# Optimization experiments

Measured on AMD Instinct MI355X. Metric: run time of the kernel, lower is better.

The kernel has to match this reference:

```python
import jax, jax.numpy as jnp
import numpy as np

WINDOW = 7
TOKEN_SELF_ATTN_VALUE = -5e4  # from lucidrains local-attention
LN_EPS = 1e-5


def _layer_norm(x, g, b):
    mu = jnp.mean(x, axis=-1, keepdims=True)
    var = jnp.mean(jnp.square(x - mu), axis=-1, keepdims=True)
    return (x - mu) * jax.lax.rsqrt(var + LN_EPS) * g + b


def _local_attention(q, k, v, window):
    # q,k,v: (b, n, d); shared_qk=True, causal=True, look_backward=1, look_forward=0
    b, n, d = q.shape
    nw = n // window
    scale = d ** -0.5
    # shared_qk: l2-normalize keys (torch F.normalize eps=1e-12)
    k = k / jnp.maximum(jnp.linalg.norm(k, axis=-1, keepdims=True), 1e-12)
    bq = q.reshape(b, nw, window, d) * scale
    bk = k.reshape(b, nw, window, d)
    bv = v.reshape(b, nw, window, d)
    # look_around: previous window + current window -> (b, nw, 2w, d)
    prev_k = jnp.pad(bk, ((0, 0), (1, 0), (0, 0), (0, 0)))[:, :nw]
    prev_v = jnp.pad(bv, ((0, 0), (1, 0), (0, 0), (0, 0)))[:, :nw]
    bk2 = jnp.concatenate([prev_k, bk], axis=2)
    bv2 = jnp.concatenate([prev_v, bv], axis=2)
    # absolute positions; padded positions marked -1
    t = jnp.arange(n).reshape(nw, window)             # (nw, w)
    prev_t = jnp.pad(t, ((1, 0), (0, 0)), constant_values=-1)[:nw]
    tk = jnp.concatenate([prev_t, t], axis=1)          # (nw, 2w)
    sim = jnp.einsum('bnie,bnje->bnij', bq, bk2)       # (b, nw, w, 2w)
    self_mask = t[:, :, None] == tk[:, None, :]
    sim = jnp.where(self_mask, TOKEN_SELF_ATTN_VALUE, sim)
    invalid = (t[:, :, None] < tk[:, None, :]) | (tk[:, None, :] == -1)
    sim = jnp.where(invalid, -jnp.finfo(sim.dtype).max, sim)
    attn = jax.nn.softmax(sim, axis=-1)
    out = jnp.einsum('bnij,bnjd->bnid', attn, bv2)
    return out.reshape(b, n, d)


def setup_inputs() -> dict:
    key = jax.random.key(0)
    ks = jax.random.split(key, 10)
    B, H, W, C = 8, 112, 112, 256
    s = 1.0 / np.sqrt(C)
    return {
        'x': jax.random.normal(ks[0], (B, H, W, C), dtype=jnp.float32),
        'ln_g': jnp.ones((C,), jnp.float32),
        'ln_b': jnp.zeros((C,), jnp.float32),
        'wq_w': jax.random.uniform(ks[1], (C, C), jnp.float32, -s, s),
        'wq_b': jax.random.uniform(ks[2], (C,), jnp.float32, -s, s),
        'wk_w': jax.random.uniform(ks[3], (C, C), jnp.float32, -s, s),
        'wk_b': jax.random.uniform(ks[4], (C,), jnp.float32, -s, s),
        'wv_w': jax.random.uniform(ks[5], (C, C), jnp.float32, -s, s),
        'wv_b': jax.random.uniform(ks[6], (C,), jnp.float32, -s, s),
        'mlp_w': jax.random.uniform(ks[7], (C, C), jnp.float32, -s, s),
        'mlp_b': jax.random.uniform(ks[8], (C,), jnp.float32, -s, s),
    }


def reference(x, ln_g, ln_b, wq_w, wq_b, wk_w, wk_b, wv_w, wv_b, mlp_w, mlp_b):
    B, H, W, C = x.shape
    shift = WINDOW // 2  # int(7/2) = 3
    xs = jnp.roll(x, (shift, shift), axis=(1, 2))
    xs = _layer_norm(xs, ln_g, ln_b)
    flat = xs.reshape(B, H * W, C)
    q = flat @ wq_w.T + wq_b
    k = flat @ wk_w.T + wk_b
    v = flat @ wv_w.T + wv_b
    attn_out = _local_attention(q, k, v, WINDOW).reshape(B, H, W, C)
    x_unshifted = jnp.roll(attn_out, (-shift, -shift), axis=(1, 2))
    residual = x_unshifted + x
    xn = _layer_norm(residual, ln_g, ln_b)  # same LN params (module reused)
    flat2 = xn.reshape(B, H * W, C)
    mlp = jax.nn.gelu(flat2 @ mlp_w.T + mlp_b, approximate=False).reshape(B, H, W, C)
    return mlp + residual
```

## Files before the change

kernel.cpp:

```cpp
#include <hip/hip_runtime.h>

#define NTOK 100352
#define NPB  12544
#define CH   256

typedef unsigned short u16;
typedef float f32x4 __attribute__((ext_vector_type(4)));
typedef short bfrag __attribute__((ext_vector_type(8)));

static __device__ __forceinline__ u16 f2bf(float f) {
    union { float f; unsigned u; } v; v.f = f;
    unsigned r = v.u + 0x7FFFu + ((v.u >> 16) & 1u);
    return (u16)(r >> 16);
}
static __device__ __forceinline__ float bf2f(u16 h) {
    union { unsigned u; float f; } v; v.u = ((unsigned)h) << 16;
    return v.f;
}
static __device__ __forceinline__ unsigned pk2(float a, float b) {
    return (unsigned)f2bf(a) | ((unsigned)f2bf(b) << 16);
}

__global__ __launch_bounds__(256)
void swa_prep(const float* __restrict__ wq, const float* __restrict__ wk,
              const float* __restrict__ wv, const float* __restrict__ wm,
              u16* __restrict__ wcat, u16* __restrict__ wmb)
{
    int i0 = blockIdx.x * 256 + threadIdx.x;
    int stride = gridDim.x * 256;
    for (int i = i0; i < 768 * 256; i += stride) {
        int r = i >> 8, c = i & 255;
        float v;
        if (r < 256)      v = wq[r * 256 + c] * 0.0625f;
        else if (r < 512) v = wk[(r - 256) * 256 + c];
        else              v = wv[(r - 512) * 256 + c];
        wcat[i] = f2bf(v);
    }
    for (int i = i0; i < 256 * 256; i += stride) wmb[i] = f2bf(wm[i]);
}

__global__ __launch_bounds__(256)
void swa_ln(const float* __restrict__ x,
            const float* __restrict__ ln_g, const float* __restrict__ ln_b,
            u16* __restrict__ xn)
{
    const int lane = threadIdx.x & 63;
    const int wid  = threadIdx.x >> 6;
    f32x4 lg = *reinterpret_cast<const f32x4*>(ln_g + lane * 4);
    f32x4 lb = *reinterpret_cast<const f32x4*>(ln_b + lane * 4);

    const int wtok0 = (blockIdx.x * 4 + wid) * 16;
    for (int i = 0; i < 16; ++i) {
        int tok = wtok0 + i;
        int b_  = tok / NPB;
        int rem = tok - b_ * NPB;
        int h = rem / 112, w = rem - h * 112;
        int h0 = h - 3 + ((h < 3) ? 112 : 0);
        int w0 = w - 3 + ((w < 3) ? 112 : 0);
        f32x4 v = *reinterpret_cast<const f32x4*>(x + (size_t)(b_ * NPB + h0 * 112 + w0) * CH + lane * 4);
        float s  = v[0] + v[1] + v[2] + v[3];
        float sq = v[0]*v[0] + v[1]*v[1] + v[2]*v[2] + v[3]*v[3];
        #pragma unroll
        for (int m = 1; m < 64; m <<= 1) { s += __shfl_xor(s, m); sq += __shfl_xor(sq, m); }
        float mu  = s * (1.0f / 256.0f);
        float var = sq * (1.0f / 256.0f) - mu * mu;
        float inv = 1.0f / sqrtf(var + 1e-5f);
        uint2 p;
        p.x = pk2((v[0] - mu) * inv * lg[0] + lb[0], (v[1] - mu) * inv * lg[1] + lb[1]);
        p.y = pk2((v[2] - mu) * inv * lg[2] + lb[2], (v[3] - mu) * inv * lg[3] + lb[3]);
        *reinterpret_cast<uint2*>(xn + (size_t)tok * CH + lane * 4) = p;
    }
}

__global__ __launch_bounds__(256)
void swa_qkv5(const u16* __restrict__ xn, const u16* __restrict__ wcat,
              const float* __restrict__ bq, const float* __restrict__ bk,
              const float* __restrict__ bv,
              u16* __restrict__ qbuf, u16* __restrict__ kbuf, u16* __restrict__ vbuf)
{
    __shared__ u16 xt[64 * 256];
    __shared__ u16 wt[2][128 * 64];

    const int tid  = threadIdx.x;
    const int lane = tid & 63;
    const int wid  = tid >> 6;
    const int r16  = lane & 15, g4 = lane >> 4;
    const int wch  = wid & 1;
    const int wtk  = wid >> 1;
    const int tkp  = (blockIdx.x & 7) * 196 + (blockIdx.x >> 3);
    const int tok0 = tkp * 64;

    char* xb = (char*)xt;

    {
        uint4 v[8];
        #pragma unroll
        for (int it = 0; it < 8; ++it) {
            int cid = tid + it * 256;
            int row = cid >> 5, c = cid & 31;
            v[it] = *reinterpret_cast<const uint4*>(xn + (size_t)(tok0 + row) * CH + c * 8);
        }
        #pragma unroll
        for (int it = 0; it < 8; ++it) {
            int cid = tid + it * 256;
            int row = cid >> 5, c = cid & 31;
            *reinterpret_cast<uint4*>(xb + row * 512 + ((c ^ (row & 7)) << 4)) = v[it];
        }
    }

    uint4 wreg[4];
    auto wload = [&](int s) {
        int chp = s >> 2, t = s & 3;
        #pragma unroll
        for (int it = 0; it < 4; ++it) {
            int cid = tid + it * 256;
            int row = cid >> 3, c = cid & 7;
            wreg[it] = *reinterpret_cast<const uint4*>(wcat + (size_t)(chp * 128 + row) * CH + t * 64 + c * 8);
        }
    };
    auto wstore = [&](int p) {
        char* d = (char*)wt[p];
        #pragma unroll
        for (int it = 0; it < 4; ++it) {
            int cid = tid + it * 256;
            int row = cid >> 3, c = cid & 7;
            *reinterpret_cast<uint4*>(d + row * 128 + ((c ^ (row & 7)) << 4)) = wreg[it];
        }
    };
    wload(0); wstore(0);
    __syncthreads();

    f32x4 acc[4][2];
    #pragma unroll
    for (int fi = 0; fi < 4; ++fi) { acc[fi][0] = (f32x4)0.f; acc[fi][1] = (f32x4)0.f; }

    for (int s = 0; s < 24; ++s) {
        const int chp = s >> 2, t = s & 3, p = s & 1;
        if (s < 23) wload(s + 1);
        const char* wp = (const char*)wt[p];
        #pragma unroll
        for (int kk = 0; kk < 2; ++kk) {
            bfrag af[4], bfj[2];
            #pragma unroll
            for (int fi = 0; fi < 4; ++fi) {
                int row = wch * 64 + fi * 16 + r16;
                af[fi] = *reinterpret_cast<const bfrag*>(wp + row * 128 + ((((kk << 2) | g4) ^ (row & 7)) << 4));
            }
            #pragma unroll
            for (int fj = 0; fj < 2; ++fj) {
                int trow = wtk * 32 + fj * 16 + r16;
                int c = t * 8 + kk * 4 + g4;
                bfj[fj] = *reinterpret_cast<const bfrag*>(xb + trow * 512 + ((c ^ (trow & 7)) << 4));
            }
            #pragma unroll
            for (int fi = 0; fi < 4; ++fi)
                #pragma unroll
                for (int fj = 0; fj < 2; ++fj)
                    acc[fi][fj] = __builtin_amdgcn_mfma_f32_16x16x32_bf16(af[fi], bfj[fj], acc[fi][fj], 0, 0, 0);
        }
        if (t == 3) {
            int sec = chp >> 1;
            u16* outp = (sec == 0) ? qbuf : (sec == 1) ? kbuf : vbuf;
            const float* bp = (sec == 0) ? bq : (sec == 1) ? bk : bv;
            float bscale = (sec == 0) ? 0.0625f : 1.0f;
            int chl0 = (chp & 1) * 128 + wch * 64;
            #pragma unroll
            for (int fi = 0; fi < 4; ++fi) {
                int chl = chl0 + fi * 16 + g4 * 4;
                f32x4 bb = *reinterpret_cast<const f32x4*>(bp + chl);
                #pragma unroll
                for (int fj = 0; fj < 2; ++fj) {
                    int tok = tok0 + wtk * 32 + fj * 16 + r16;
                    uint2 pk;
                    pk.x = pk2(acc[fi][fj][0] + bb[0] * bscale, acc[fi][fj][1] + bb[1] * bscale);
                    pk.y = pk2(acc[fi][fj][2] + bb[2] * bscale, acc[fi][fj][3] + bb[3] * bscale);
                    *reinterpret_cast<uint2*>(outp + (size_t)tok * CH + chl) = pk;
                    acc[fi][fj] = (f32x4)0.f;
                }
            }
        }
        if (s < 23) wstore(p ^ 1);
        __syncthreads();
    }
}

__global__ __launch_bounds__(256)
void swa_attn(const u16* qbuf, const u16* kbuf, const u16* vbuf, u16* obuf)
{
    __shared__ float plds[4][16][17];
    const int tid  = threadIdx.x;
    const int lane = tid & 63;
    const int wid  = tid >> 6;
    const int win  = blockIdx.x * 4 + wid;
    const int iw   = win % 1792;
    const int base = win * 7;
    const int r16  = lane & 15;
    const int g4   = lane >> 4;

    int qrow = base + r16; if (qrow > NTOK - 1) qrow = NTOK - 1;
    int krow = base - 7 + r16; if (krow < 0) krow = 0;
    const u16* qp = qbuf + (size_t)qrow * CH + g4 * 8;
    const u16* kp = kbuf + (size_t)krow * CH + g4 * 8;

    bfrag kf[8];
    #pragma unroll
    for (int kk = 0; kk < 8; ++kk) kf[kk] = *reinterpret_cast<const bfrag*>(kp + kk * 32);
    float sq = 0.f;
    #pragma unroll
    for (int kk = 0; kk < 8; ++kk)
        #pragma unroll
        for (int e = 0; e < 8; ++e) { float kv = bf2f((u16)kf[kk][e]); sq += kv * kv; }
    sq += __shfl_xor(sq, 16); sq += __shfl_xor(sq, 32);
    float invk = 1.0f / fmaxf(sqrtf(sq), 1e-12f);

    f32x4 s4 = {0.f, 0.f, 0.f, 0.f};
    #pragma unroll
    for (int kk = 0; kk < 8; ++kk) {
        bfrag a = *reinterpret_cast<const bfrag*>(qp + kk * 32);
        s4 = __builtin_amdgcn_mfma_f32_16x16x32_bf16(a, kf[kk], s4, 0, 0, 0);
    }

    const int  j     = r16;
    const bool first = (iw == 0);
    #pragma unroll
    for (int rr = 0; rr < 4; ++rr) {
        int i = g4 * 4 + rr;
        float s = s4[rr] * invk;
        if (j == i + 7) s = -5.0e4f;
        if (j > i + 7 || j >= 14 || (first && j < 7)) s = -3.0e38f;
        s4[rr] = s;
    }
    f32x4 mx = s4;
    #pragma unroll
    for (int off = 8; off; off >>= 1) {
        #pragma unroll
        for (int rr = 0; rr < 4; ++rr) mx[rr] = fmaxf(mx[rr], __shfl_xor(mx[rr], off));
    }
    f32x4 p;
    #pragma unroll
    for (int rr = 0; rr < 4; ++rr) p[rr] = __expf(s4[rr] - mx[rr]);
    f32x4 sm = p;
    #pragma unroll
    for (int off = 8; off; off >>= 1) {
        #pragma unroll
        for (int rr = 0; rr < 4; ++rr) sm[rr] += __shfl_xor(sm[rr], off);
    }
    #pragma unroll
    for (int rr = 0; rr < 4; ++rr) plds[wid][g4 * 4 + rr][j] = p[rr] / sm[rr];
    __syncthreads();

    f32x4 zero4 = {0.f, 0.f, 0.f, 0.f};
    f32x4 oa[7];
    #pragma unroll
    for (int i = 0; i < 7; ++i) oa[i] = zero4;
    for (int jj = 0; jj < 14; ++jj) {
        int vrow = base - 7 + jj;
        if (vrow < 0) vrow = 0;
        ushort4 vr = *reinterpret_cast<const ushort4*>(vbuf + (size_t)vrow * CH + lane * 4);
        f32x4 vvv; vvv[0] = bf2f(vr.x); vvv[1] = bf2f(vr.y); vvv[2] = bf2f(vr.z); vvv[3] = bf2f(vr.w);
        #pragma unroll
        for (int i = 0; i < 7; ++i) {
            float pp = plds[wid][i][jj];
            oa[i][0] += pp * vvv[0]; oa[i][1] += pp * vvv[1];
            oa[i][2] += pp * vvv[2]; oa[i][3] += pp * vvv[3];
        }
    }
    #pragma unroll
    for (int i = 0; i < 7; ++i) {
        ushort4 o; o.x = f2bf(oa[i][0]); o.y = f2bf(oa[i][1]); o.z = f2bf(oa[i][2]); o.w = f2bf(oa[i][3]);
        *reinterpret_cast<ushort4*>(obuf + (size_t)(base + i) * CH + lane * 4) = o;
    }
}

__global__ __launch_bounds__(256)
void swa_mlp4(const float* __restrict__ x, const u16* __restrict__ abuf,
              const float* __restrict__ ln_g, const float* __restrict__ ln_b,
              const u16* __restrict__ wmb, const float* __restrict__ mbias,
              float* __restrict__ out)
{
    __shared__ u16   xs[32][264];
    __shared__ float rsd[32][260];
    __shared__ float bias[256];
    const int tid  = threadIdx.x;
    const int lane = tid & 63;
    const int wid  = tid >> 6;
    const int tok0 = blockIdx.x * 32;
    const int r16  = lane & 15;
    const int g4   = lane >> 4;

    if (tid < 256) bias[tid] = mbias[tid];
    f32x4 lg = *reinterpret_cast<const f32x4*>(ln_g + lane * 4);
    f32x4 lb = *reinterpret_cast<const f32x4*>(ln_b + lane * 4);

    for (int it = 0; it < 8; ++it) {
        int tt  = wid * 8 + it;
        int tok = tok0 + tt;
        int b_  = tok / NPB, rem = tok - b_ * NPB;
        int h = rem / 112, w = rem - h * 112;
        int hs = h + 3;  if (hs >= 112) hs -= 112;
        int ws_ = w + 3; if (ws_ >= 112) ws_ -= 112;
        const u16* arow = abuf + (size_t)(b_ * NPB + hs * 112 + ws_) * CH;
        ushort4 av = *reinterpret_cast<const ushort4*>(arow + lane * 4);
        f32x4 xv = *reinterpret_cast<const f32x4*>(x + (size_t)tok * CH + lane * 4);
        f32x4 rv;
        rv[0] = xv[0] + bf2f(av.x); rv[1] = xv[1] + bf2f(av.y);
        rv[2] = xv[2] + bf2f(av.z); rv[3] = xv[3] + bf2f(av.w);
        *reinterpret_cast<f32x4*>(&rsd[tt][lane * 4]) = rv;
        float s  = rv[0] + rv[1] + rv[2] + rv[3];
        float sq = rv[0]*rv[0] + rv[1]*rv[1] + rv[2]*rv[2] + rv[3]*rv[3];
        #pragma unroll
        for (int m = 32; m; m >>= 1) { s += __shfl_xor(s, m); sq += __shfl_xor(sq, m); }
        float mu  = s * (1.0f / 256.0f);
        float var = sq * (1.0f / 256.0f) - mu * mu;
        float inv = 1.0f / sqrtf(var + 1e-5f);
        ushort4 o;
        o.x = f2bf((rv[0] - mu) * inv * lg[0] + lb[0]);
        o.y = f2bf((rv[1] - mu) * inv * lg[1] + lb[1]);
        o.z = f2bf((rv[2] - mu) * inv * lg[2] + lb[2]);
        o.w = f2bf((rv[3] - mu) * inv * lg[3] + lb[3]);
        *reinterpret_cast<ushort4*>(&xs[tt][lane * 4]) = o;
    }
    __syncthreads();

    f32x4 acc[4][2];
    #pragma unroll
    for (int i = 0; i < 4; ++i) { acc[i][0] = (f32x4)0.f; acc[i][1] = (f32x4)0.f; }

    #pragma unroll
    for (int kk = 0; kk < 8; ++kk) {
        bfrag b0 = *reinterpret_cast<const bfrag*>(&xs[r16][kk * 32 + g4 * 8]);
        bfrag b1 = *reinterpret_cast<const bfrag*>(&xs[16 + r16][kk * 32 + g4 * 8]);
        #pragma unroll
        for (int ct = 0; ct < 4; ++ct) {
            bfrag wf = *reinterpret_cast<const bfrag*>(wmb + (size_t)(wid * 64 + ct * 16 + r16) * CH + kk * 32 + g4 * 8);
            acc[ct][0] = __builtin_amdgcn_mfma_f32_16x16x32_bf16(wf, b0, acc[ct][0], 0, 0, 0);
            acc[ct][1] = __builtin_amdgcn_mfma_f32_16x16x32_bf16(wf, b1, acc[ct][1], 0, 0, 0);
        }
    }

    #pragma unroll
    for (int ct = 0; ct < 4; ++ct) {
        int ch = wid * 64 + ct * 16 + g4 * 4;
        f32x4 bb = *reinterpret_cast<const f32x4*>(&bias[ch]);
        #pragma unroll
        for (int rt = 0; rt < 2; ++rt) {
            int tokL = rt * 16 + r16;
            f32x4 rb = *reinterpret_cast<const f32x4*>(&rsd[tokL][ch]);
            f32x4 vv;
            #pragma unroll
            for (int rr = 0; rr < 4; ++rr) {
                float val = acc[ct][rt][rr] + bb[rr];
                vv[rr] = 0.5f * val * (1.0f + erff(val * 0.70710678118654752f)) + rb[rr];
            }
            *reinterpret_cast<f32x4*>(out + (size_t)(tok0 + tokL) * CH + ch) = vv;
        }
    }
}

extern "C" void kernel_launch(void* const* d_in, const int* in_sizes, int n_in,
                              void* d_out, int out_size, void* d_ws, size_t ws_size,
                              hipStream_t stream)
{
    const float* x     = (const float*)d_in[0];
    const float* ln_g  = (const float*)d_in[1];
    const float* ln_b  = (const float*)d_in[2];
    const float* wq_w  = (const float*)d_in[3];
    const float* wq_b  = (const float*)d_in[4];
    const float* wk_w  = (const float*)d_in[5];
    const float* wk_b  = (const float*)d_in[6];
    const float* wv_w  = (const float*)d_in[7];
    const float* wv_b  = (const float*)d_in[8];
    const float* mlp_w = (const float*)d_in[9];
    const float* mlp_b = (const float*)d_in[10];

    char* ws = (char*)d_ws;
    u16* wcat = (u16*)ws;
    u16* wmb  = (u16*)(ws + 393216);
    u16* xnq  = (u16*)(ws + 524288);
    u16* kbuf = (u16*)d_out;
    u16* vbuf = (u16*)d_out + (size_t)NTOK * CH;

    swa_prep <<<256,  256, 0, stream>>>(wq_w, wk_w, wv_w, mlp_w, wcat, wmb);
    swa_ln   <<<1568, 256, 0, stream>>>(x, ln_g, ln_b, xnq);
    swa_qkv5 <<<1568, 256, 0, stream>>>(xnq, wcat, wq_b, wk_b, wv_b, xnq, kbuf, vbuf);
    swa_attn <<<3584, 256, 0, stream>>>(xnq, kbuf, vbuf, xnq);
    swa_mlp4 <<<3136, 256, 0, stream>>>(x, xnq, ln_g, ln_b, wmb, mlp_b, (float*)d_out);
}
```

Before: 310.4 us.

## Keep QKV activation tiles in registers and double tokens per block

The QKV projection kernel now gives each block 128 tokens instead of 64. Each wave loads its own 32-token slice of the normalized input straight into registers as MFMA B-fragments, so the 32 KB LDS activation tile and its staging are gone. Weights are streamed as 64x64 bf16 tiles, double-buffered through LDS over 48 steps. This halves the weight traffic and the LDS footprint per token, at the cost of more VGPRs, more barriers per block and fewer blocks in the grid.

Measured after the change: 305.2 us. About the same (-1.7%).

```diff
diff --git a/kernel.cpp b/kernel.cpp
--- a/kernel.cpp
+++ b/kernel.cpp
@@ -73,60 +73,50 @@
 }
 
 __global__ __launch_bounds__(256)
-void swa_qkv5(const u16* __restrict__ xn, const u16* __restrict__ wcat,
+void swa_qkv6(const u16* __restrict__ xn, const u16* __restrict__ wcat,
               const float* __restrict__ bq, const float* __restrict__ bk,
               const float* __restrict__ bv,
               u16* __restrict__ qbuf, u16* __restrict__ kbuf, u16* __restrict__ vbuf)
 {
-    __shared__ u16 xt[64 * 256];
-    __shared__ u16 wt[2][128 * 64];
+    __shared__ u16 wt[2][64 * 64];
 
     const int tid  = threadIdx.x;
     const int lane = tid & 63;
     const int wid  = tid >> 6;
     const int r16  = lane & 15, g4 = lane >> 4;
-    const int wch  = wid & 1;
-    const int wtk  = wid >> 1;
-    const int tkp  = (blockIdx.x & 7) * 196 + (blockIdx.x >> 3);
-    const int tok0 = tkp * 64;
-
-    char* xb = (char*)xt;
-
-    {
-        uint4 v[8];
-        #pragma unroll
-        for (int it = 0; it < 8; ++it) {
-            int cid = tid + it * 256;
-            int row = cid >> 5, c = cid & 31;
-            v[it] = *reinterpret_cast<const uint4*>(xn + (size_t)(tok0 + row) * CH + c * 8);
-        }
-        #pragma unroll
-        for (int it = 0; it < 8; ++it) {
-            int cid = tid + it * 256;
-            int row = cid >> 5, c = cid & 31;
-            *reinterpret_cast<uint4*>(xb + row * 512 + ((c ^ (row & 7)) << 4)) = v[it];
-        }
-    }
-
-    uint4 wreg[4];
+    const int swz  = (blockIdx.x & 7) * 98 + (blockIdx.x >> 3);
+    const int tok0 = swz * 128;
+    const int trow0 = wid * 32;
+
+    bfrag bx[2][8];
+    #pragma unroll
+    for (int fj = 0; fj < 2; ++fj) {
+        const u16* xp = xn + (size_t)(tok0 + trow0 + fj * 16 + r16) * CH + g4 * 8;
+        #pragma unroll
+        for (int kk = 0; kk < 8; ++kk)
+            bx[fj][kk] = *reinterpret_cast<const bfrag*>(xp + kk * 32);
+    }
+
+    uint4 wreg[2];
     auto wload = [&](int s) {
-        int chp = s >> 2, t = s & 3;
-        #pragma unroll
-        for (int it = 0; it < 4; ++it) {
+        int pp = s >> 2, t = s & 3;
+        #pragma unroll
+        for (int it = 0; it < 2; ++it) {
             int cid = tid + it * 256;
             int row = cid >> 3, c = cid & 7;
-            wreg[it] = *reinterpret_cast<const uint4*>(wcat + (size_t)(chp * 128 + row) * CH + t * 64 + c * 8);
+            wreg[it] = *reinterpret_cast<const uint4*>(wcat + (size_t)(pp * 64 + row) * CH + t * 64 + c * 8);
         }
     };
     auto wstore = [&](int p) {
         char* d = (char*)wt[p];
         #pragma unroll
-        for (int it = 0; it < 4; ++it) {
+        for (int it = 0; it < 2; ++it) {
             int cid = tid + it * 256;
             int row = cid >> 3, c = cid & 7;
             *reinterpret_cast<uint4*>(d + row * 128 + ((c ^ (row & 7)) << 4)) = wreg[it];
         }
     };
+
     wload(0); wstore(0);
     __syncthreads();
 
@@ -134,53 +124,50 @@
     #pragma unroll
     for (int fi = 0; fi < 4; ++fi) { acc[fi][0] = (f32x4)0.f; acc[fi][1] = (f32x4)0.f; }
 
-    for (int s = 0; s < 24; ++s) {
-        const int chp = s >> 2, t = s & 3, p = s & 1;
-        if (s < 23) wload(s + 1);
-        const char* wp = (const char*)wt[p];
-        #pragma unroll
-        for (int kk = 0; kk < 2; ++kk) {
-            bfrag af[4], bfj[2];
+    for (int pp = 0; pp < 12; ++pp) {
+        #pragma unroll
+        for (int t = 0; t < 4; ++t) {
+            const int s = pp * 4 + t;
+            const int p = s & 1;
+            if (s < 47) wload(s + 1);
+            const char* wp = (const char*)wt[p];
             #pragma unroll
-            for (int fi = 0; fi < 4; ++fi) {
-                int row = wch * 64 + fi * 16 + r16;
-                af[fi] = *reinterpret_cast<const bfrag*>(wp + row * 128 + ((((kk << 2) | g4) ^ (row & 7)) << 4));
+            for (int kk = 0; kk < 2; ++kk) {
+                bfrag af[4];
+                #pragma unroll
+                for (int fi = 0; fi < 4; ++fi) {
+                    int row = fi * 16 + r16;
+                    af[fi] = *reinterpret_cast<const bfrag*>(wp + row * 128 + (((kk * 4 + g4) ^ (row & 7)) << 4));
+                }
+                #pragma unroll
+                for (int fi = 0; fi < 4; ++fi)
+                    #pragma unroll
+                    for (int fj = 0; fj < 2; ++fj)
+                        acc[fi][fj] = __builtin_amdgcn_mfma_f32_16x16x32_bf16(af[fi], bx[fj][t * 2 + kk], acc[fi][fj], 0, 0, 0);
             }
-            #pragma unroll
-            for (int fj = 0; fj < 2; ++fj) {
-                int trow = wtk * 32 + fj * 16 + r16;
-                int c = t * 8 + kk * 4 + g4;
-                bfj[fj] = *reinterpret_cast<const bfrag*>(xb + trow * 512 + ((c ^ (trow & 7)) << 4));
-            }
-            #pragma unroll
-            for (int fi = 0; fi < 4; ++fi)
+            if (t == 3) {
+                const int sec = pp >> 2;
+                u16* outp = (sec == 0) ? qbuf : (sec == 1) ? kbuf : vbuf;
+                const float* bp = (sec == 0) ? bq : (sec == 1) ? bk : bv;
+                const float bscale = (sec == 0) ? 0.0625f : 1.0f;
                 #pragma unroll
-                for (int fj = 0; fj < 2; ++fj)
-                    acc[fi][fj] = __builtin_amdgcn_mfma_f32_16x16x32_bf16(af[fi], bfj[fj], acc[fi][fj], 0, 0, 0);
-        }
-        if (t == 3) {
-            int sec = chp >> 1;
-            u16* outp = (sec == 0) ? qbuf : (sec == 1) ? kbuf : vbuf;
-            const float* bp = (sec == 0) ? bq : (sec == 1) ? bk : bv;
-            float bscale = (sec == 0) ? 0.0625f : 1.0f;
-            int chl0 = (chp & 1) * 128 + wch * 64;
-            #pragma unroll
-            for (int fi = 0; fi < 4; ++fi) {
-                int chl = chl0 + fi * 16 + g4 * 4;
-                f32x4 bb = *reinterpret_cast<const f32x4*>(bp + chl);
-                #pragma unroll
-                for (int fj = 0; fj < 2; ++fj) {
-                    int tok = tok0 + wtk * 32 + fj * 16 + r16;
-                    uint2 pk;
-                    pk.x = pk2(acc[fi][fj][0] + bb[0] * bscale, acc[fi][fj][1] + bb[1] * bscale);
-                    pk.y = pk2(acc[fi][fj][2] + bb[2] * bscale, acc[fi][fj][3] + bb[3] * bscale);
-                    *reinterpret_cast<uint2*>(outp + (size_t)tok * CH + chl) = pk;
-                    acc[fi][fj] = (f32x4)0.f;
+                for (int fi = 0; fi < 4; ++fi) {
+                    int chl = (pp & 3) * 64 + fi * 16 + g4 * 4;
+                    f32x4 bb = *reinterpret_cast<const f32x4*>(bp + chl);
+                    #pragma unroll
+                    for (int fj = 0; fj < 2; ++fj) {
+                        int tok = tok0 + trow0 + fj * 16 + r16;
+                        uint2 pk;
+                        pk.x = pk2(acc[fi][fj][0] + bb[0] * bscale, acc[fi][fj][1] + bb[1] * bscale);
+                        pk.y = pk2(acc[fi][fj][2] + bb[2] * bscale, acc[fi][fj][3] + bb[3] * bscale);
+                        *reinterpret_cast<uint2*>(outp + (size_t)tok * CH + chl) = pk;
+                        acc[fi][fj] = (f32x4)0.f;
+                    }
                 }
             }
-        }
-        if (s < 23) wstore(p ^ 1);
-        __syncthreads();
+            if (s < 47) wstore(p ^ 1);
+            __syncthreads();
+        }
     }
 }
 
@@ -382,7 +369,7 @@
 
     swa_prep <<<256,  256, 0, stream>>>(wq_w, wk_w, wv_w, mlp_w, wcat, wmb);
     swa_ln   <<<1568, 256, 0, stream>>>(x, ln_g, ln_b, xnq);
-    swa_qkv5 <<<1568, 256, 0, stream>>>(xnq, wcat, wq_b, wk_b, wv_b, xnq, kbuf, vbuf);
+    swa_qkv6 <<<784,  256, 0, stream>>>(xnq, wcat, wq_b, wk_b, wv_b, xnq, kbuf, vbuf);
     swa_attn <<<3584, 256, 0, stream>>>(xnq, kbuf, vbuf, xnq);
     swa_mlp4 <<<3136, 256, 0, stream>>>(x, xnq, ln_g, ln_b, wmb, mlp_b, (float*)d_out);
 }
```
